# Performance work log

Measured on AMD Instinct MI355X. Metric: run time of the kernel, lower is better.

Reference implementation:

```python
import jax, jax.numpy as jnp
import numpy as np

B, S, D, H = 4, 2048, 1024, 16
DK = D // H  # 64


def setup_inputs() -> dict:
    key = jax.random.key(0)
    ks = jax.random.split(key, 5)
    scale = 1.0 / np.sqrt(D)
    return {
        "embeddings": jax.random.normal(ks[0], (B, S, D), dtype=jnp.float32),
        "W_q": jax.random.normal(ks[1], (D, D), dtype=jnp.float32) * scale,
        "W_k": jax.random.normal(ks[2], (D, D), dtype=jnp.float32) * scale,
        "W_v": jax.random.normal(ks[3], (D, D), dtype=jnp.float32) * scale,
        "W_o": jax.random.normal(ks[4], (D, D), dtype=jnp.float32) * scale,
    }


def reference(embeddings, W_q, W_k, W_v, W_o):
    # torch nn.Linear: y = x @ W.T  (weights are [out, in])
    b, s, d = embeddings.shape
    h, dk = H, DK
    q = embeddings @ W_q.T  # [b, s, d]
    k = embeddings @ W_k.T
    v = embeddings @ W_v.T
    # split heads along last dim (matches the per-head slicing in the torch loop)
    q = q.reshape(b, s, h, dk)
    k = k.reshape(b, s, h, dk)
    v = v.reshape(b, s, h, dk)
    scores = jnp.einsum("bqhd,bkhd->bhqk", q, k) / jnp.sqrt(jnp.float32(dk))
    p = jax.nn.softmax(scores, axis=-1)  # dropout is identity at eval
    ctx = jnp.einsum("bhqk,bkhd->bqhd", p, v).reshape(b, s, d)
    return ctx @ W_o.T
```

## Files before the change

### kernel.cpp

```cpp
#include <hip/hip_runtime.h>
#include <hip/hip_bf16.h>

typedef unsigned short u16;
typedef __attribute__((ext_vector_type(8))) short bf16x8;
typedef __attribute__((ext_vector_type(4))) float f32x4;
typedef __attribute__((ext_vector_type(2))) unsigned int u32x2;

#define AS1 __attribute__((address_space(1)))
#define AS3 __attribute__((address_space(3)))

constexpr int Bc = 4, Sc = 2048, Dc = 1024, Hc = 16, DKc = 64;
constexpr size_t EDc = (size_t)Bc * Sc * Dc;
constexpr size_t WDc = (size_t)Dc * Dc;

__device__ __forceinline__ void g2l16(const void* g, void* l) {
  __builtin_amdgcn_global_load_lds((const AS1 unsigned int*)g,
                                   (AS3 unsigned int*)l, 16, 0, 0);
}

__device__ __forceinline__ u16 f2b(float f) {
  union { float f; unsigned u; } x; x.f = f;
  unsigned r = x.u + 0x7fffu + ((x.u >> 16) & 1u);
  return (u16)(r >> 16);
}

#if __has_builtin(__builtin_amdgcn_cvt_pk_bf16_f32)
typedef __attribute__((ext_vector_type(2))) __bf16 hbf2;
__device__ __forceinline__ unsigned f2b_pk(float a, float b) {
  union { hbf2 v; unsigned u; } x;
  x.v = __builtin_amdgcn_cvt_pk_bf16_f32(a, b);
  return x.u;
}
#else
__device__ __forceinline__ unsigned f2b_pk(float a, float b) {
  return (unsigned)f2b(a) | ((unsigned)f2b(b) << 16);
}
#endif

__device__ __forceinline__ float fast_exp2(float x) {
#if __has_builtin(__builtin_amdgcn_exp2f)
  return __builtin_amdgcn_exp2f(x);
#else
  return exp2f(x);
#endif
}

__global__ __launch_bounds__(256)
void cvt_all(const float* __restrict__ e, const float* __restrict__ wq,
             const float* __restrict__ wk, const float* __restrict__ wv,
             const float* __restrict__ wo, u16* __restrict__ dst) {
  int bx = blockIdx.x;
  const float* src;
  size_t doff;
  int chunk;
  if (bx < 4096) {
    src = e; doff = 0; chunk = bx;
  } else {
    int t = bx - 4096;
    int w = t >> 9;
    chunk = t & 511;
    src = (w == 0) ? wq : (w == 1) ? wk : (w == 2) ? wv : wo;
    doff = EDc + (size_t)w * WDc;
  }
  size_t i = ((size_t)chunk * 256 + threadIdx.x) * 8;
  float4 a = *(const float4*)(src + i);
  float4 b = *(const float4*)(src + i + 4);
  bf16x8 o;
  o[0] = (short)f2b(a.x); o[1] = (short)f2b(a.y);
  o[2] = (short)f2b(a.z); o[3] = (short)f2b(a.w);
  o[4] = (short)f2b(b.x); o[5] = (short)f2b(b.y);
  o[6] = (short)f2b(b.z); o[7] = (short)f2b(b.w);
  *(bf16x8*)(dst + doff + i) = o;
}

__global__ __launch_bounds__(256, 2)
void gemm_qkv(const u16* __restrict__ X, const u16* __restrict__ Wq,
              const u16* __restrict__ Wk, const u16* __restrict__ Wv,
              u16* __restrict__ Qo, u16* __restrict__ Ko,
              u16* __restrict__ VTo) {
  constexpr int BM = 128, BK = 64, K = Dc, N = Dc;
  __shared__ u16 As[BM * BK];
  __shared__ u16 Bs[BM * BK];

  const int tid = threadIdx.x;
  const int wave = tid >> 6, lane = tid & 63;
  const int mr = lane & 15, quad = lane >> 4, mr7 = lane & 7;
  const int sect = blockIdx.x >> 3;
  const int n0 = (blockIdx.x & 7) * 128;
  const int m0 = blockIdx.y * BM;
  const u16* W = (sect == 0) ? Wq : (sect == 1) ? Wk : Wv;
  const int wm = (wave >> 1) * 64, wn = (wave & 1) * 64;
  const int ldr = lane >> 3;
  const int ldc_sw = ((lane & 7) ^ (ldr & 7)) * 8;
  const bool vsec = (sect == 2);

  const f32x4 zero = {0.f, 0.f, 0.f, 0.f};
  f32x4 acc[4][4];
  #pragma unroll
  for (int i = 0; i < 4; i++)
    #pragma unroll
    for (int j = 0; j < 4; j++) acc[i][j] = zero;

  for (int k0 = 0; k0 < K; k0 += BK) {
    __syncthreads();
    #pragma unroll
    for (int i = 0; i < 4; i++) {
      int row = wave * 32 + i * 8;
      g2l16(X + (size_t)(m0 + row + ldr) * K + k0 + ldc_sw, As + row * BK);
      g2l16(W + (size_t)(n0 + row + ldr) * K + k0 + ldc_sw, Bs + row * BK);
    }
    __syncthreads();

    #pragma unroll
    for (int c = 0; c < 2; c++) {
      bf16x8 a[4], b[4];
      #pragma unroll
      for (int i = 0; i < 4; i++)
        a[i] = *(const bf16x8*)(As + (wm + i * 16 + mr) * BK +
                                (((c * 4 + quad) ^ mr7) * 8));
      #pragma unroll
      for (int j = 0; j < 4; j++)
        b[j] = *(const bf16x8*)(Bs + (wn + j * 16 + mr) * BK +
                                (((c * 4 + quad) ^ mr7) * 8));
      if (vsec) {
        #pragma unroll
        for (int i = 0; i < 4; i++)
          #pragma unroll
          for (int j = 0; j < 4; j++)
            acc[i][j] = __builtin_amdgcn_mfma_f32_16x16x32_bf16(
                b[j], a[i], acc[i][j], 0, 0, 0);
      } else {
        #pragma unroll
        for (int i = 0; i < 4; i++)
          #pragma unroll
          for (int j = 0; j < 4; j++)
            acc[i][j] = __builtin_amdgcn_mfma_f32_16x16x32_bf16(
                a[i], b[j], acc[i][j], 0, 0, 0);
      }
    }
  }

  if (vsec) {
    #pragma unroll
    for (int i = 0; i < 4; i++) {
      int s_glob = m0 + wm + i * 16 + mr;
      int bb = s_glob >> 11, s = s_glob & 2047;
      #pragma unroll
      for (int j = 0; j < 4; j++) {
        int nbase = n0 + wn + j * 16 + quad * 4;
        #pragma unroll
        for (int r = 0; r < 4; r++) {
          int n = nbase + r;
          int h = n >> 6, d = n & 63;
          VTo[((size_t)((bb * Hc + h) * DKc + d)) * Sc + s] = f2b(acc[i][j][r]);
        }
      }
    }
  } else {
    const float scale = (sect == 0) ? 0.18033688f : 1.0f;
    u16* Y = (sect == 0) ? Qo : Ko;
    #pragma unroll
    for (int i = 0; i < 4; i++)
      #pragma unroll
      for (int j = 0; j < 4; j++)
        #pragma unroll
        for (int r = 0; r < 4; r++) {
          int m = m0 + wm + i * 16 + quad * 4 + r;
          int n = n0 + wn + j * 16 + mr;
          Y[(size_t)m * N + n] = f2b(acc[i][j][r] * scale);
        }
  }
}

__global__ __launch_bounds__(256, 2)
void gemm_out(const u16* __restrict__ X, const u16* __restrict__ W,
              float* __restrict__ Y, int M, int N, int K) {
  constexpr int BM = 128, BK = 64;
  __shared__ u16 As[BM * BK];
  __shared__ u16 Bs[BM * BK];

  const int tid = threadIdx.x;
  const int wave = tid >> 6, lane = tid & 63;
  const int mr = lane & 15, quad = lane >> 4, mr7 = lane & 7;
  const int m0 = blockIdx.y * BM, n0 = blockIdx.x * BM;
  const int wm = (wave >> 1) * 64, wn = (wave & 1) * 64;
  const int ldr = lane >> 3;
  const int ldc_sw = ((lane & 7) ^ (ldr & 7)) * 8;

  const f32x4 zero = {0.f, 0.f, 0.f, 0.f};
  f32x4 acc[4][4];
  #pragma unroll
  for (int i = 0; i < 4; i++)
    #pragma unroll
    for (int j = 0; j < 4; j++) acc[i][j] = zero;

  for (int k0 = 0; k0 < K; k0 += BK) {
    __syncthreads();
    #pragma unroll
    for (int i = 0; i < 4; i++) {
      int row = wave * 32 + i * 8;
      g2l16(X + (size_t)(m0 + row + ldr) * K + k0 + ldc_sw, As + row * BK);
      g2l16(W + (size_t)(n0 + row + ldr) * K + k0 + ldc_sw, Bs + row * BK);
    }
    __syncthreads();

    #pragma unroll
    for (int c = 0; c < 2; c++) {
      bf16x8 a[4], b[4];
      #pragma unroll
      for (int i = 0; i < 4; i++)
        a[i] = *(const bf16x8*)(As + (wm + i * 16 + mr) * BK +
                                (((c * 4 + quad) ^ mr7) * 8));
      #pragma unroll
      for (int j = 0; j < 4; j++)
        b[j] = *(const bf16x8*)(Bs + (wn + j * 16 + mr) * BK +
                                (((c * 4 + quad) ^ mr7) * 8));
      #pragma unroll
      for (int i = 0; i < 4; i++)
        #pragma unroll
        for (int j = 0; j < 4; j++)
          acc[i][j] = __builtin_amdgcn_mfma_f32_16x16x32_bf16(
              a[i], b[j], acc[i][j], 0, 0, 0);
    }
  }

  #pragma unroll
  for (int i = 0; i < 4; i++)
    #pragma unroll
    for (int j = 0; j < 4; j++)
      #pragma unroll
      for (int r = 0; r < 4; r++) {
        int m = m0 + wm + i * 16 + quad * 4 + r;
        int n = n0 + wn + j * 16 + mr;
        Y[(size_t)m * N + n] = acc[i][j][r];
      }
}

__global__ __launch_bounds__(256, 2)
void attn(const u16* __restrict__ Q, const u16* __restrict__ K,
          const u16* __restrict__ VT, u16* __restrict__ O) {
  __shared__ u16 Ks[2][64 * 64];
  __shared__ u16 Vs[2][64 * 64];
  __shared__ u16 Ps[16][16 * 64];

  const int tid = threadIdx.x;
  const int wave = tid >> 6, lane = tid & 63;
  const int mr = lane & 15, quad = lane >> 4, mr7 = lane & 7;
  const int bh = blockIdx.y;
  const int b = bh >> 4, h = bh & 15;
  const int q0 = blockIdx.x * 256;
  const size_t headK = (size_t)b * Sc * Dc + (size_t)h * DKc;
  const size_t headV = (size_t)bh * DKc * Sc;
  const int ldr = lane >> 3;
  const int ldc_sw = ((lane & 7) ^ (ldr & 7)) * 8;

  const int row0a = wave * 16, row0b = wave * 16 + 8;
  const int pa_r = row0a + ldr, pb_r = row0b + ldr;
  const int sra = ((pa_r & 15) << 2) | (pa_r >> 4);
  const int srb = ((pb_r & 15) << 2) | (pb_r >> 4);

  bf16x8 qa[4][2];
  #pragma unroll
  for (int sub = 0; sub < 4; sub++)
    #pragma unroll
    for (int c = 0; c < 2; c++)
      qa[sub][c] = *(const bf16x8*)(Q + headK +
          (size_t)(q0 + wave * 64 + sub * 16 + mr) * Dc + c * 32 + quad * 8);

  const f32x4 zero = {0.f, 0.f, 0.f, 0.f};
  f32x4 o[4][4];
  float lrow[4][4];
  #pragma unroll
  for (int sub = 0; sub < 4; sub++)
    #pragma unroll
    for (int i = 0; i < 4; i++) {
      o[sub][i] = zero;
      lrow[sub][i] = 0.f;
    }

  {
    const u16* Kb_ = K + headK;
    const u16* Vb_ = VT + headV;
    g2l16(Kb_ + (size_t)sra * Dc + ldc_sw, Ks[0] + row0a * 64);
    g2l16(Kb_ + (size_t)srb * Dc + ldc_sw, Ks[0] + row0b * 64);
    g2l16(Vb_ + (size_t)(row0a + ldr) * Sc + ldc_sw, Vs[0] + row0a * 64);
    g2l16(Vb_ + (size_t)(row0b + ldr) * Sc + ldc_sw, Vs[0] + row0b * 64);
  }
  __syncthreads();

  for (int kt = 0; kt < Sc / 64; kt++) {
    const int cur = kt & 1;
    if (kt + 1 < Sc / 64) {
      const int nk0 = (kt + 1) * 64;
      const int nxt = cur ^ 1;
      g2l16(K + headK + (size_t)(nk0 + sra) * Dc + ldc_sw, Ks[nxt] + row0a * 64);
      g2l16(K + headK + (size_t)(nk0 + srb) * Dc + ldc_sw, Ks[nxt] + row0b * 64);
      g2l16(VT + headV + (size_t)(row0a + ldr) * Sc + nk0 + ldc_sw, Vs[nxt] + row0a * 64);
      g2l16(VT + headV + (size_t)(row0b + ldr) * Sc + nk0 + ldc_sw, Vs[nxt] + row0b * 64);
    }

    bf16x8 kb[4][2];
    #pragma unroll
    for (int kc = 0; kc < 4; kc++)
      #pragma unroll
      for (int c = 0; c < 2; c++)
        kb[kc][c] = *(const bf16x8*)(Ks[cur] + (kc * 16 + mr) * 64 +
                                     (((c * 4 + quad) ^ mr7) * 8));

    #pragma unroll
    for (int sub = 0; sub < 4; sub++) {
      f32x4 s[4];
      #pragma unroll
      for (int kc = 0; kc < 4; kc++) {
        s[kc] = zero;
        #pragma unroll
        for (int c = 0; c < 2; c++)
          s[kc] = __builtin_amdgcn_mfma_f32_16x16x32_bf16(
              qa[sub][c], kb[kc][c], s[kc], 0, 0, 0);
      }
      u16* Pw = Ps[wave * 4 + sub];
      #pragma unroll
      for (int r = 0; r < 4; r++) {
        float p0 = fast_exp2(s[0][r]);
        float p1 = fast_exp2(s[1][r]);
        float p2 = fast_exp2(s[2][r]);
        float p3 = fast_exp2(s[3][r]);
        lrow[sub][r] += (p0 + p1) + (p2 + p3);
        u32x2 w;
        w.x = f2b_pk(p0, p1);
        w.y = f2b_pk(p2, p3);
        *(u32x2*)(Pw + (quad * 4 + r) * 64 + mr * 4) = w;
      }
    }

    bf16x8 vb[4][2];
    #pragma unroll
    for (int ni = 0; ni < 4; ni++)
      #pragma unroll
      for (int c = 0; c < 2; c++)
        vb[ni][c] = *(const bf16x8*)(Vs[cur] + (ni * 16 + mr) * 64 +
                                     (((c * 4 + quad) ^ mr7) * 8));

    #pragma unroll
    for (int sub = 0; sub < 4; sub++) {
      const u16* Pw = Ps[wave * 4 + sub];
      bf16x8 pa0 = *(const bf16x8*)(Pw + mr * 64 + quad * 8);
      bf16x8 pa1 = *(const bf16x8*)(Pw + mr * 64 + 32 + quad * 8);
      #pragma unroll
      for (int ni = 0; ni < 4; ni++) {
        o[sub][ni] = __builtin_amdgcn_mfma_f32_16x16x32_bf16(
            pa0, vb[ni][0], o[sub][ni], 0, 0, 0);
        o[sub][ni] = __builtin_amdgcn_mfma_f32_16x16x32_bf16(
            pa1, vb[ni][1], o[sub][ni], 0, 0, 0);
      }
    }

    __syncthreads();
  }

  #pragma unroll
  for (int sub = 0; sub < 4; sub++)
    #pragma unroll
    for (int r = 0; r < 4; r++) {
      float l = lrow[sub][r];
      #pragma unroll
      for (int off = 1; off < 16; off <<= 1)
        l += __shfl_xor(l, off, 64);
      float inv = 1.0f / l;
      #pragma unroll
      for (int ni = 0; ni < 4; ni++) {
        int qq = q0 + wave * 64 + sub * 16 + quad * 4 + r;
        O[headK + (size_t)qq * Dc + ni * 16 + mr] = f2b(o[sub][ni][r] * inv);
      }
    }
}

extern "C" void kernel_launch(void* const* d_in, const int* in_sizes, int n_in,
                              void* d_out, int out_size, void* d_ws, size_t ws_size,
                              hipStream_t stream) {
  const float* emb = (const float*)d_in[0];
  const float* Wq  = (const float*)d_in[1];
  const float* Wk  = (const float*)d_in[2];
  const float* Wv  = (const float*)d_in[3];
  const float* Wo  = (const float*)d_in[4];
  float* out = (float*)d_out;

  const int M = Bc * Sc;

  u16* Eb  = (u16*)d_ws;
  u16* Wqb = Eb  + EDc;
  u16* Wkb = Wqb + WDc;
  u16* Wvb = Wkb + WDc;
  u16* Wob = Wvb + WDc;
  u16* Qb  = Wob + WDc;
  u16* Kb  = Qb  + EDc;
  u16* VTb = Kb  + EDc;
  u16* Cb  = Qb;

  dim3 blk(256);
  cvt_all<<<dim3(4096 + 4 * 512), blk, 0, stream>>>(emb, Wq, Wk, Wv, Wo, Eb);

  gemm_qkv<<<dim3(24, M / 128), blk, 0, stream>>>(Eb, Wqb, Wkb, Wvb,
                                                  Qb, Kb, VTb);

  attn<<<dim3(Sc / 256, Bc * Hc), blk, 0, stream>>>(Qb, Kb, VTb, Cb);

  gemm_out<<<dim3(Dc / 128, M / 128), blk, 0, stream>>>(Cb, Wob, out,
                                                        M, Dc, Dc);
}
```

Baseline: 272.6 us.

## Keep softmax probabilities in registers via transposed QK^T and permuted V layout

Computes S^T by swapping MFMA operands so each lane holds a row of probabilities laid out as the A operand for the PV MFMA. This removes the LDS round trip for P. V^T is stored with a permuted sequence index in the projection epilogue so the register layout matches, and the K row permutation is dropped. It also adds s_setprio around MFMA bursts and simplifies the row-sum reduction. The risk is correctness of the index permutation and higher register pressure.

```diff
diff --git a/kernel.cpp b/kernel.cpp
--- a/kernel.cpp
+++ b/kernel.cpp
@@ -4,7 +4,6 @@
 typedef unsigned short u16;
 typedef __attribute__((ext_vector_type(8))) short bf16x8;
 typedef __attribute__((ext_vector_type(4))) float f32x4;
-typedef __attribute__((ext_vector_type(2))) unsigned int u32x2;
 
 #define AS1 __attribute__((address_space(1)))
 #define AS3 __attribute__((address_space(3)))
@@ -145,6 +144,8 @@
     for (int i = 0; i < 4; i++) {
       int s_glob = m0 + wm + i * 16 + mr;
       int bb = s_glob >> 11, s = s_glob & 2047;
+      int sp = (s & ~63) | (s & 32) | ((s & 12) << 1) | ((s & 16) >> 2) |
+               (s & 3);
       #pragma unroll
       for (int j = 0; j < 4; j++) {
         int nbase = n0 + wn + j * 16 + quad * 4;
@@ -152,7 +153,7 @@
         for (int r = 0; r < 4; r++) {
           int n = nbase + r;
           int h = n >> 6, d = n & 63;
-          VTo[((size_t)((bb * Hc + h) * DKc + d)) * Sc + s] = f2b(acc[i][j][r]);
+          VTo[((size_t)((bb * Hc + h) * DKc + d)) * Sc + sp] = f2b(acc[i][j][r]);
         }
       }
     }
@@ -241,7 +242,6 @@
           const u16* __restrict__ VT, u16* __restrict__ O) {
   __shared__ u16 Ks[2][64 * 64];
   __shared__ u16 Vs[2][64 * 64];
-  __shared__ u16 Ps[16][16 * 64];
 
   const int tid = threadIdx.x;
   const int wave = tid >> 6, lane = tid & 63;
@@ -256,8 +256,6 @@
 
   const int row0a = wave * 16, row0b = wave * 16 + 8;
   const int pa_r = row0a + ldr, pb_r = row0b + ldr;
-  const int sra = ((pa_r & 15) << 2) | (pa_r >> 4);
-  const int srb = ((pb_r & 15) << 2) | (pb_r >> 4);
 
   bf16x8 qa[4][2];
   #pragma unroll
@@ -269,34 +267,31 @@
 
   const f32x4 zero = {0.f, 0.f, 0.f, 0.f};
   f32x4 o[4][4];
-  float lrow[4][4];
-  #pragma unroll
-  for (int sub = 0; sub < 4; sub++)
-    #pragma unroll
-    for (int i = 0; i < 4; i++) {
-      o[sub][i] = zero;
-      lrow[sub][i] = 0.f;
-    }
-
-  {
-    const u16* Kb_ = K + headK;
-    const u16* Vb_ = VT + headV;
-    g2l16(Kb_ + (size_t)sra * Dc + ldc_sw, Ks[0] + row0a * 64);
-    g2l16(Kb_ + (size_t)srb * Dc + ldc_sw, Ks[0] + row0b * 64);
-    g2l16(Vb_ + (size_t)(row0a + ldr) * Sc + ldc_sw, Vs[0] + row0a * 64);
-    g2l16(Vb_ + (size_t)(row0b + ldr) * Sc + ldc_sw, Vs[0] + row0b * 64);
-  }
+  float lsum[4];
+  #pragma unroll
+  for (int sub = 0; sub < 4; sub++) {
+    lsum[sub] = 0.f;
+    #pragma unroll
+    for (int i = 0; i < 4; i++) o[sub][i] = zero;
+  }
+
+  g2l16(K + headK + (size_t)pa_r * Dc + ldc_sw, Ks[0] + row0a * 64);
+  g2l16(K + headK + (size_t)pb_r * Dc + ldc_sw, Ks[0] + row0b * 64);
+  g2l16(VT + headV + (size_t)pa_r * Sc + ldc_sw, Vs[0] + row0a * 64);
+  g2l16(VT + headV + (size_t)pb_r * Sc + ldc_sw, Vs[0] + row0b * 64);
   __syncthreads();
+
+  union W8 { unsigned u[4]; bf16x8 v; };
 
   for (int kt = 0; kt < Sc / 64; kt++) {
     const int cur = kt & 1;
     if (kt + 1 < Sc / 64) {
       const int nk0 = (kt + 1) * 64;
       const int nxt = cur ^ 1;
-      g2l16(K + headK + (size_t)(nk0 + sra) * Dc + ldc_sw, Ks[nxt] + row0a * 64);
-      g2l16(K + headK + (size_t)(nk0 + srb) * Dc + ldc_sw, Ks[nxt] + row0b * 64);
-      g2l16(VT + headV + (size_t)(row0a + ldr) * Sc + nk0 + ldc_sw, Vs[nxt] + row0a * 64);
-      g2l16(VT + headV + (size_t)(row0b + ldr) * Sc + nk0 + ldc_sw, Vs[nxt] + row0b * 64);
+      g2l16(K + headK + (size_t)(nk0 + pa_r) * Dc + ldc_sw, Ks[nxt] + row0a * 64);
+      g2l16(K + headK + (size_t)(nk0 + pb_r) * Dc + ldc_sw, Ks[nxt] + row0b * 64);
+      g2l16(VT + headV + (size_t)pa_r * Sc + nk0 + ldc_sw, Vs[nxt] + row0a * 64);
+      g2l16(VT + headV + (size_t)pb_r * Sc + nk0 + ldc_sw, Vs[nxt] + row0b * 64);
     }
 
     bf16x8 kb[4][2];
@@ -307,30 +302,38 @@
         kb[kc][c] = *(const bf16x8*)(Ks[cur] + (kc * 16 + mr) * 64 +
                                      (((c * 4 + quad) ^ mr7) * 8));
 
+    W8 paw[4][2];
     #pragma unroll
     for (int sub = 0; sub < 4; sub++) {
       f32x4 s[4];
+      __builtin_amdgcn_s_setprio(1);
       #pragma unroll
       for (int kc = 0; kc < 4; kc++) {
-        s[kc] = zero;
-        #pragma unroll
-        for (int c = 0; c < 2; c++)
-          s[kc] = __builtin_amdgcn_mfma_f32_16x16x32_bf16(
-              qa[sub][c], kb[kc][c], s[kc], 0, 0, 0);
+        s[kc] = __builtin_amdgcn_mfma_f32_16x16x32_bf16(
+            kb[kc][0], qa[sub][0], zero, 0, 0, 0);
+        s[kc] = __builtin_amdgcn_mfma_f32_16x16x32_bf16(
+            kb[kc][1], qa[sub][1], s[kc], 0, 0, 0);
       }
-      u16* Pw = Ps[wave * 4 + sub];
-      #pragma unroll
-      for (int r = 0; r < 4; r++) {
-        float p0 = fast_exp2(s[0][r]);
-        float p1 = fast_exp2(s[1][r]);
-        float p2 = fast_exp2(s[2][r]);
-        float p3 = fast_exp2(s[3][r]);
-        lrow[sub][r] += (p0 + p1) + (p2 + p3);
-        u32x2 w;
-        w.x = f2b_pk(p0, p1);
-        w.y = f2b_pk(p2, p3);
-        *(u32x2*)(Pw + (quad * 4 + r) * 64 + mr * 4) = w;
-      }
+      __builtin_amdgcn_s_setprio(0);
+      float e[16];
+      #pragma unroll
+      for (int kc = 0; kc < 4; kc++)
+        #pragma unroll
+        for (int r = 0; r < 4; r++)
+          e[kc * 4 + r] = fast_exp2(s[kc][r]);
+      float acc0 = (e[0] + e[1]) + (e[2] + e[3]);
+      float acc1 = (e[4] + e[5]) + (e[6] + e[7]);
+      float acc2 = (e[8] + e[9]) + (e[10] + e[11]);
+      float acc3 = (e[12] + e[13]) + (e[14] + e[15]);
+      lsum[sub] += (acc0 + acc1) + (acc2 + acc3);
+      paw[sub][0].u[0] = f2b_pk(e[0], e[1]);
+      paw[sub][0].u[1] = f2b_pk(e[2], e[3]);
+      paw[sub][0].u[2] = f2b_pk(e[4], e[5]);
+      paw[sub][0].u[3] = f2b_pk(e[6], e[7]);
+      paw[sub][1].u[0] = f2b_pk(e[8], e[9]);
+      paw[sub][1].u[1] = f2b_pk(e[10], e[11]);
+      paw[sub][1].u[2] = f2b_pk(e[12], e[13]);
+      paw[sub][1].u[3] = f2b_pk(e[14], e[15]);
     }
 
     bf16x8 vb[4][2];
@@ -343,36 +346,34 @@
 
     #pragma unroll
     for (int sub = 0; sub < 4; sub++) {
-      const u16* Pw = Ps[wave * 4 + sub];
-      bf16x8 pa0 = *(const bf16x8*)(Pw + mr * 64 + quad * 8);
-      bf16x8 pa1 = *(const bf16x8*)(Pw + mr * 64 + 32 + quad * 8);
+      __builtin_amdgcn_s_setprio(1);
       #pragma unroll
       for (int ni = 0; ni < 4; ni++) {
         o[sub][ni] = __builtin_amdgcn_mfma_f32_16x16x32_bf16(
-            pa0, vb[ni][0], o[sub][ni], 0, 0, 0);
+            paw[sub][0].v, vb[ni][0], o[sub][ni], 0, 0, 0);
         o[sub][ni] = __builtin_amdgcn_mfma_f32_16x16x32_bf16(
-            pa1, vb[ni][1], o[sub][ni], 0, 0, 0);
+            paw[sub][1].v, vb[ni][1], o[sub][ni], 0, 0, 0);
       }
+      __builtin_amdgcn_s_setprio(0);
     }
 
     __syncthreads();
   }
 
   #pragma unroll
-  for (int sub = 0; sub < 4; sub++)
+  for (int sub = 0; sub < 4; sub++) {
+    float l = lsum[sub];
+    l += __shfl_xor(l, 16, 64);
+    l += __shfl_xor(l, 32, 64);
     #pragma unroll
     for (int r = 0; r < 4; r++) {
-      float l = lrow[sub][r];
-      #pragma unroll
-      for (int off = 1; off < 16; off <<= 1)
-        l += __shfl_xor(l, off, 64);
-      float inv = 1.0f / l;
-      #pragma unroll
-      for (int ni = 0; ni < 4; ni++) {
-        int qq = q0 + wave * 64 + sub * 16 + quad * 4 + r;
+      float inv = 1.0f / __shfl(l, quad * 4 + r, 64);
+      int qq = q0 + wave * 64 + sub * 16 + quad * 4 + r;
+      #pragma unroll
+      for (int ni = 0; ni < 4; ni++)
         O[headK + (size_t)qq * Dc + ni * 16 + mr] = f2b(o[sub][ni][r] * inv);
-      }
-    }
+    }
+  }
 }
 
 extern "C" void kernel_launch(void* const* d_in, const int* in_sizes, int n_in,
```

Measured after the change: 268.2 us. No clear change (-1.6%).
